# Optimization experiments

Measured on AMD Instinct MI355X. Metric: run time of the kernel, lower is better.

## Reference

```python
import jax, jax.numpy as jnp
import numpy as np


def _gcn_conv(x, W, b, src, dst, n):
    """PyG GCNConv: linear transform, then symmetric-normalized scatter-add.
    src/dst already include self-loops. deg computed over dst (col), matching PyG."""
    h = x @ W                                           # [N, C_out]
    deg = jax.ops.segment_sum(jnp.ones(dst.shape, h.dtype), dst, num_segments=n)
    dinv = jnp.where(deg > 0, deg ** -0.5, 0.0)         # deg^-1/2, inf -> 0
    norm = dinv[src] * dinv[dst]                        # [E+N]
    msg = h[src] * norm[:, None]                        # gather + scale
    return jax.ops.segment_sum(msg, dst, num_segments=n) + b


def setup_inputs() -> dict:
    key = jax.random.key(0)
    k1, k2, k3, k4 = jax.random.split(key, 4)
    N, E, F_IN, F_HID, F_OUT = 100000, 1600000, 128, 128, 128
    x = jax.random.normal(k1, (N, F_IN), dtype=jnp.float32)
    W1 = jax.random.normal(k2, (F_IN, F_HID), dtype=jnp.float32) * (1.0 / np.sqrt(F_IN))
    b1 = jnp.zeros((F_HID,), dtype=jnp.float32)
    W2 = jax.random.normal(k3, (F_HID, F_OUT), dtype=jnp.float32) * (1.0 / np.sqrt(F_HID))
    b2 = jnp.zeros((F_OUT,), dtype=jnp.float32)
    edge_index = jax.random.randint(k4, (2, E), 0, N, dtype=jnp.int64)
    return {"x": x, "W1": W1, "b1": b1, "W2": W2, "b2": b2, "edge_index": edge_index}


def reference(x, W1, b1, W2, b2, edge_index):
    n = x.shape[0]
    loops = jnp.arange(n, dtype=edge_index.dtype)       # add self-loops (PyG default)
    src = jnp.concatenate([edge_index[0], loops])
    dst = jnp.concatenate([edge_index[1], loops])
    h = jax.nn.relu(_gcn_conv(x, W1, b1, src, dst, n))
    out = jax.nn.relu(_gcn_conv(h, W2, b2, src, dst, n))
    return out
```

## Files before the change

kernel.cpp:

```cpp
#include <hip/hip_runtime.h>

#define TPB 256
#define CHA 8192

typedef _Float16 half_t;
typedef _Float16 half4 __attribute__((ext_vector_type(4)));
typedef _Float16 half8 __attribute__((ext_vector_type(8)));
typedef float f32x4 __attribute__((ext_vector_type(4)));

__global__ __launch_bounds__(512) void k_binA(unsigned* __restrict__ keys,
                                              int* __restrict__ bcursor,
                                              const int* __restrict__ ei,
                                              long long E, int NB, int CAP) {
  __shared__ int hist[512];
  __shared__ int scanv[512];
  __shared__ int base_run[512];
  __shared__ int bump[512];
  __shared__ unsigned stage[CHA];

  const int tid = threadIdx.x;
  const long long e0 = (long long)blockIdx.x * CHA;
  const int cnt_here = (int)min((long long)CHA, E - e0);

  hist[tid] = 0; bump[tid] = 0;
  __syncthreads();

  for (int i = tid; i < cnt_here; i += 512)
    atomicAdd(&hist[ei[E + e0 + i] >> 8], 1);
  __syncthreads();

  int v = hist[tid];
  scanv[tid] = v;
  __syncthreads();
  for (int ofs = 1; ofs < 512; ofs <<= 1) {
    int t = (tid >= ofs) ? scanv[tid - ofs] : 0;
    __syncthreads();
    scanv[tid] += t;
    __syncthreads();
  }
  scanv[tid] -= v;
  if (tid < NB) {
    int c = hist[tid];
    base_run[tid] = c ? atomicAdd(&bcursor[tid], c) : 0;
  }
  __syncthreads();

  for (int i = tid; i < cnt_here; i += 512) {
    int s = ei[e0 + i];
    int d = ei[E + e0 + i];
    int b = d >> 8;
    int r = atomicAdd(&bump[b], 1);
    stage[scanv[b] + r] = ((unsigned)s << 8) | (unsigned)(d & 255);
  }
  __syncthreads();

  const int wave = tid >> 6, lane = tid & 63;
  for (int b = wave; b < NB; b += 8) {
    int s0 = scanv[b], c = hist[b], rb = base_run[b];
    long long gbase = (long long)b * CAP + rb;
    int cmax = min(c, CAP - rb);
    for (int j = lane; j < cmax; j += 64) keys[gbase + j] = stage[s0 + j];
  }
}

__global__ __launch_bounds__(TPB) void k_binB(int* __restrict__ pay,
                                              int* __restrict__ cnt,
                                              int* __restrict__ off,
                                              float* __restrict__ dinv,
                                              const unsigned* __restrict__ keys,
                                              const int* __restrict__ bcursor,
                                              int N, int CAP) {
  __shared__ int lcnt[256], lofs[256], lcur[256];
  const int tid = threadIdx.x;
  const int b = blockIdx.x;
  const long long lo = (long long)b * CAP;
  const int total = min(bcursor[b], CAP);

  lcnt[tid] = 0; lcur[tid] = 0;
  __syncthreads();
  for (int i = tid; i < total; i += TPB)
    atomicAdd(&lcnt[keys[lo + i] & 255], 1);
  __syncthreads();

  int v = lcnt[tid];
  lofs[tid] = v;
  __syncthreads();
  for (int ofs = 1; ofs < 256; ofs <<= 1) {
    int t = (tid >= ofs) ? lofs[tid - ofs] : 0;
    __syncthreads();
    lofs[tid] += t;
    __syncthreads();
  }
  lofs[tid] -= v;
  __syncthreads();

  const int node = (b << 8) + tid;
  if (node < N) {
    cnt[node] = v;
    off[node] = (int)lo + lofs[tid];
    dinv[node] = rsqrtf(1.0f + (float)v);
  }

  for (int i = tid; i < total; i += TPB) {
    unsigned k = keys[lo + i];
    int l = (int)(k & 255u);
    int r = atomicAdd(&lcur[l], 1);
    pay[lo + lofs[l] + r] = (int)(k >> 8);
  }
}

__global__ __launch_bounds__(TPB) void k_prepW(half_t* __restrict__ Wf1,
                                               const float* __restrict__ W1,
                                               half_t* __restrict__ Wf2,
                                               const float* __restrict__ W2) {
  int gid = blockIdx.x * TPB + threadIdx.x;
  int f = gid & 4095;
  const float* W = (gid < 4096) ? W1 : W2;
  half_t* Wf = (gid < 4096) ? Wf1 : Wf2;
  int j0 = (f & 1) * 4;
  int lane = (f >> 1) & 63;
  int nt = (f >> 7) & 7;
  int kc = f >> 10;
  int n = nt * 16 + (lane & 15);
  int kb = kc * 32 + ((lane >> 4) << 3) + j0;
  half4 o;
  o.x = (_Float16)W[(kb + 0) * 128 + n];
  o.y = (_Float16)W[(kb + 1) * 128 + n];
  o.z = (_Float16)W[(kb + 2) * 128 + n];
  o.w = (_Float16)W[(kb + 3) * 128 + n];
  *(half4*)&Wf[f * 4] = o;
}

template <int AF16>
__global__ __launch_bounds__(TPB) void k_gemm_mfma(const void* __restrict__ Ain,
                                                   const half_t* __restrict__ Wf,
                                                   const float* __restrict__ dinv,
                                                   half_t* __restrict__ hs, int N) {
  __shared__ half_t As[128 * 128];
  __shared__ half_t Ws[16384];
  const int tid = threadIdx.x;
  const long long row0 = (long long)blockIdx.x * 128;

  {
    half8* d = (half8*)Ws;
    const half8* s = (const half8*)Wf;
#pragma unroll
    for (int i = 0; i < 8; ++i) d[i * 256 + tid] = s[i * 256 + tid];
  }
  {
#pragma unroll
    for (int i = 0; i < 8; ++i) {
      int s = i * 256 + tid;
      int lane6 = s & 63;
      int grp = s >> 6;
      int mtile = grp >> 2, kc = grp & 3;
      int m = lane6 & 15, kg = lane6 >> 4;
      long long gr = row0 + mtile * 16 + m;
      half8 hv = {};
      if (gr < (long long)N) {
        if (AF16) {
          hv = ((const half8*)Ain)[gr * 16 + kc * 4 + kg];
        } else {
          const float4* A4 = (const float4*)Ain;
          float4 v0 = A4[gr * 32 + kc * 8 + kg * 2];
          float4 v1 = A4[gr * 32 + kc * 8 + kg * 2 + 1];
          hv[0] = (_Float16)v0.x; hv[1] = (_Float16)v0.y;
          hv[2] = (_Float16)v0.z; hv[3] = (_Float16)v0.w;
          hv[4] = (_Float16)v1.x; hv[5] = (_Float16)v1.y;
          hv[6] = (_Float16)v1.z; hv[7] = (_Float16)v1.w;
        }
      }
      ((half8*)As)[s] = hv;
    }
  }
  __syncthreads();

  const int rg = tid >> 6, lane = tid & 63;
  f32x4 acc0[8], acc1[8];
#pragma unroll
  for (int nt = 0; nt < 8; ++nt) {
    f32x4 z = {0.f, 0.f, 0.f, 0.f};
    acc0[nt] = z; acc1[nt] = z;
  }
#pragma unroll
  for (int kc = 0; kc < 4; ++kc) {
    half8 a0 = ((const half8*)As)[((rg * 2 + 0) * 4 + kc) * 64 + lane];
    half8 a1 = ((const half8*)As)[((rg * 2 + 1) * 4 + kc) * 64 + lane];
#pragma unroll
    for (int nt = 0; nt < 8; ++nt) {
      half8 b = ((const half8*)Ws)[(kc * 8 + nt) * 64 + lane];
      acc0[nt] = __builtin_amdgcn_mfma_f32_16x16x32_f16(a0, b, acc0[nt], 0, 0, 0);
      acc1[nt] = __builtin_amdgcn_mfma_f32_16x16x32_f16(a1, b, acc1[nt], 0, 0, 0);
    }
  }

  const int ncol = lane & 15;
  const int mbase = (lane >> 4) << 2;
#pragma unroll
  for (int mt = 0; mt < 2; ++mt) {
#pragma unroll
    for (int r = 0; r < 4; ++r) {
      long long grow = row0 + (rg * 2 + mt) * 16 + mbase + r;
      if (grow < (long long)N) {
        float sc = dinv[grow];
        half_t* dst = &hs[grow * 128 + ncol];
#pragma unroll
        for (int nt = 0; nt < 8; ++nt)
          dst[nt * 16] =
              (_Float16)(((mt == 0) ? acc0[nt][r] : acc1[nt][r]) * sc);
      }
    }
  }
}

template <int OUTF16>
__global__ __launch_bounds__(TPB) void k_agg(void* __restrict__ outp,
                                             const half4* __restrict__ hs,
                                             const int* __restrict__ pay,
                                             const int* __restrict__ off,
                                             const int* __restrict__ cnt,
                                             const float* __restrict__ dinv,
                                             const float4* __restrict__ b, int N) {
  long long t = (long long)blockIdx.x * TPB + threadIdx.x;
  int g = (int)(t >> 5);
  if (g >= N) return;
  int c = (int)(t & 31);
  float di = dinv[g];
  float4 bv = b[c];

  half4 hv = hs[(long long)g * 32 + c];
  float4 acc;
  acc.x = (float)hv.x; acc.y = (float)hv.y;
  acc.z = (float)hv.z; acc.w = (float)hv.w;

  int p = off[g];
  const int en = p + cnt[g];

  for (; p + 8 <= en; p += 8) {
    int s[8];
#pragma unroll
    for (int u = 0; u < 8; ++u) s[u] = pay[p + u];
    half4 v[8];
#pragma unroll
    for (int u = 0; u < 8; ++u) v[u] = hs[(long long)s[u] * 32 + c];
#pragma unroll
    for (int u = 0; u < 8; ++u) {
      acc.x += (float)v[u].x; acc.y += (float)v[u].y;
      acc.z += (float)v[u].z; acc.w += (float)v[u].w;
    }
  }
  if (p + 4 <= en) {
    int s[4];
#pragma unroll
    for (int u = 0; u < 4; ++u) s[u] = pay[p + u];
    half4 v[4];
#pragma unroll
    for (int u = 0; u < 4; ++u) v[u] = hs[(long long)s[u] * 32 + c];
#pragma unroll
    for (int u = 0; u < 4; ++u) {
      acc.x += (float)v[u].x; acc.y += (float)v[u].y;
      acc.z += (float)v[u].z; acc.w += (float)v[u].w;
    }
    p += 4;
  }
  for (; p < en; ++p) {
    half4 v = hs[(long long)pay[p] * 32 + c];
    acc.x += (float)v.x; acc.y += (float)v.y;
    acc.z += (float)v.z; acc.w += (float)v.w;
  }

  float4 o;
  o.x = fmaxf(fmaf(acc.x, di, bv.x), 0.f);
  o.y = fmaxf(fmaf(acc.y, di, bv.y), 0.f);
  o.z = fmaxf(fmaf(acc.z, di, bv.z), 0.f);
  o.w = fmaxf(fmaf(acc.w, di, bv.w), 0.f);

  if (OUTF16) {
    half4 ho;
    ho.x = (_Float16)o.x; ho.y = (_Float16)o.y;
    ho.z = (_Float16)o.z; ho.w = (_Float16)o.w;
    ((half4*)outp)[(long long)g * 32 + c] = ho;
  } else {
    ((float4*)outp)[(long long)g * 32 + c] = o;
  }
}


extern "C" void kernel_launch(void* const* d_in, const int* in_sizes, int n_in,
                              void* d_out, int out_size, void* d_ws, size_t ws_size,
                              hipStream_t stream) {
  const float* x  = (const float*)d_in[0];
  const float* W1 = (const float*)d_in[1];
  const float* b1 = (const float*)d_in[2];
  const float* W2 = (const float*)d_in[3];
  const float* b2 = (const float*)d_in[4];
  const int*   ei = (const int*)d_in[5];

  const int N = in_sizes[0] / 128;
  const long long E = in_sizes[5] / 2;
  const int NB = (N + 255) >> 8;

  int CAP = (int)(((2 * (E / NB) + 255) / 256) * 256);
  if (CAP < 4096) CAP = 4096;

  char* w = (char*)d_ws;
  half_t*   hs      = (half_t*)w;          w += (size_t)N * 128 * 2;
  half_t*   a1h     = (half_t*)w;          w += (size_t)N * 128 * 2;
  int*      pay     = (int*)w;             w += (size_t)NB * CAP * 4;
  unsigned* keys    = (unsigned*)w;        w += (size_t)NB * CAP * 4;
  int*      cnt     = (int*)w;             w += (size_t)N * 4;
  int*      off     = (int*)w;             w += (size_t)N * 4;
  float*    dinv    = (float*)w;           w += (size_t)N * 4;
  half_t*   Wf1     = (half_t*)w;          w += 16384 * 2;
  half_t*   Wf2     = (half_t*)w;          w += 16384 * 2;
  int*      bcursor = (int*)w;

  float* out = (float*)d_out;

  const long long n32 = (long long)N * 32;
  const int gN32 = (int)((n32 + TPB - 1) / TPB);
  const int gGemm = (N + 127) / 128;
  const int gBinA = (int)((E + CHA - 1) / CHA);

  k_prepW<<<32, TPB, 0, stream>>>(Wf1, W1, Wf2, W2);

  hipMemsetAsync(bcursor, 0, (size_t)NB * 4, stream);
  k_binA<<<gBinA, 512, 0, stream>>>(keys, bcursor, ei, E, NB, CAP);
  k_binB<<<NB, TPB, 0, stream>>>(pay, cnt, off, dinv, keys, bcursor, N, CAP);

  k_gemm_mfma<0><<<gGemm, TPB, 0, stream>>>(x, Wf1, dinv, hs, N);
  k_agg<1><<<gN32, TPB, 0, stream>>>(a1h, (const half4*)hs, pay, off,
                                     cnt, dinv, (const float4*)b1, N);

  k_gemm_mfma<1><<<gGemm, TPB, 0, stream>>>(a1h, Wf2, dinv, hs, N);
  k_agg<0><<<gN32, TPB, 0, stream>>>(out, (const half4*)hs, pay, off,
                                     cnt, dinv, (const float4*)b2, N);
}
```

Measured before the change: 211.9 us.

## Fuse weight prep into binning, drop LDS staging, add nontemporal loads/stores

Merges the weight-conversion kernel into the edge-binning kernel as extra blocks, which removes one launch. The binning kernel no longer does the shared-memory prefix scan and staging; each edge key is written straight to its global bucket slot. Nontemporal loads and stores are added on streaming data in binB, the GEMM input read, and the aggregation kernel, so that streamed data does not evict the reused hs gather rows from cache. Writing keys directly trades coalesced writes for scattered ones, and dropping the large LDS buffer should allow more binA blocks per CU.

```diff
diff --git a/kernel.cpp b/kernel.cpp
--- a/kernel.cpp
+++ b/kernel.cpp
@@ -11,14 +11,38 @@
 __global__ __launch_bounds__(512) void k_binA(unsigned* __restrict__ keys,
                                               int* __restrict__ bcursor,
                                               const int* __restrict__ ei,
-                                              long long E, int NB, int CAP) {
+                                              long long E, int NB, int CAP,
+                                              int gBinA,
+                                              half_t* __restrict__ Wf1,
+                                              const float* __restrict__ W1,
+                                              half_t* __restrict__ Wf2,
+                                              const float* __restrict__ W2) {
+  const int tid = threadIdx.x;
+
+  if (blockIdx.x >= gBinA) {
+    int gid = (blockIdx.x - gBinA) * 512 + tid;
+    int f = gid & 4095;
+    const float* W = (gid < 4096) ? W1 : W2;
+    half_t* Wf = (gid < 4096) ? Wf1 : Wf2;
+    int j0 = (f & 1) * 4;
+    int lane = (f >> 1) & 63;
+    int nt = (f >> 7) & 7;
+    int kc = f >> 10;
+    int n = nt * 16 + (lane & 15);
+    int kb = kc * 32 + ((lane >> 4) << 3) + j0;
+    half4 o;
+    o.x = (_Float16)W[(kb + 0) * 128 + n];
+    o.y = (_Float16)W[(kb + 1) * 128 + n];
+    o.z = (_Float16)W[(kb + 2) * 128 + n];
+    o.w = (_Float16)W[(kb + 3) * 128 + n];
+    *(half4*)&Wf[f * 4] = o;
+    return;
+  }
+
   __shared__ int hist[512];
-  __shared__ int scanv[512];
   __shared__ int base_run[512];
   __shared__ int bump[512];
-  __shared__ unsigned stage[CHA];
-
-  const int tid = threadIdx.x;
+
   const long long e0 = (long long)blockIdx.x * CHA;
   const int cnt_here = (int)min((long long)CHA, E - e0);
 
@@ -29,16 +53,6 @@
     atomicAdd(&hist[ei[E + e0 + i] >> 8], 1);
   __syncthreads();
 
-  int v = hist[tid];
-  scanv[tid] = v;
-  __syncthreads();
-  for (int ofs = 1; ofs < 512; ofs <<= 1) {
-    int t = (tid >= ofs) ? scanv[tid - ofs] : 0;
-    __syncthreads();
-    scanv[tid] += t;
-    __syncthreads();
-  }
-  scanv[tid] -= v;
   if (tid < NB) {
     int c = hist[tid];
     base_run[tid] = c ? atomicAdd(&bcursor[tid], c) : 0;
@@ -49,17 +63,9 @@
     int s = ei[e0 + i];
     int d = ei[E + e0 + i];
     int b = d >> 8;
-    int r = atomicAdd(&bump[b], 1);
-    stage[scanv[b] + r] = ((unsigned)s << 8) | (unsigned)(d & 255);
-  }
-  __syncthreads();
-
-  const int wave = tid >> 6, lane = tid & 63;
-  for (int b = wave; b < NB; b += 8) {
-    int s0 = scanv[b], c = hist[b], rb = base_run[b];
-    long long gbase = (long long)b * CAP + rb;
-    int cmax = min(c, CAP - rb);
-    for (int j = lane; j < cmax; j += 64) keys[gbase + j] = stage[s0 + j];
+    int r = base_run[b] + atomicAdd(&bump[b], 1);
+    if (r < CAP)
+      keys[(long long)b * CAP + r] = ((unsigned)s << 8) | (unsigned)(d & 255);
   }
 }
 
@@ -79,7 +85,7 @@
   lcnt[tid] = 0; lcur[tid] = 0;
   __syncthreads();
   for (int i = tid; i < total; i += TPB)
-    atomicAdd(&lcnt[keys[lo + i] & 255], 1);
+    atomicAdd(&lcnt[__builtin_nontemporal_load(&keys[lo + i]) & 255], 1);
   __syncthreads();
 
   int v = lcnt[tid];
@@ -107,28 +113,6 @@
     int r = atomicAdd(&lcur[l], 1);
     pay[lo + lofs[l] + r] = (int)(k >> 8);
   }
-}
-
-__global__ __launch_bounds__(TPB) void k_prepW(half_t* __restrict__ Wf1,
-                                               const float* __restrict__ W1,
-                                               half_t* __restrict__ Wf2,
-                                               const float* __restrict__ W2) {
-  int gid = blockIdx.x * TPB + threadIdx.x;
-  int f = gid & 4095;
-  const float* W = (gid < 4096) ? W1 : W2;
-  half_t* Wf = (gid < 4096) ? Wf1 : Wf2;
-  int j0 = (f & 1) * 4;
-  int lane = (f >> 1) & 63;
-  int nt = (f >> 7) & 7;
-  int kc = f >> 10;
-  int n = nt * 16 + (lane & 15);
-  int kb = kc * 32 + ((lane >> 4) << 3) + j0;
-  half4 o;
-  o.x = (_Float16)W[(kb + 0) * 128 + n];
-  o.y = (_Float16)W[(kb + 1) * 128 + n];
-  o.z = (_Float16)W[(kb + 2) * 128 + n];
-  o.w = (_Float16)W[(kb + 3) * 128 + n];
-  *(half4*)&Wf[f * 4] = o;
 }
 
 template <int AF16>
@@ -161,13 +145,14 @@
         if (AF16) {
           hv = ((const half8*)Ain)[gr * 16 + kc * 4 + kg];
         } else {
-          const float4* A4 = (const float4*)Ain;
-          float4 v0 = A4[gr * 32 + kc * 8 + kg * 2];
-          float4 v1 = A4[gr * 32 + kc * 8 + kg * 2 + 1];
-          hv[0] = (_Float16)v0.x; hv[1] = (_Float16)v0.y;
-          hv[2] = (_Float16)v0.z; hv[3] = (_Float16)v0.w;
-          hv[4] = (_Float16)v1.x; hv[5] = (_Float16)v1.y;
-          hv[6] = (_Float16)v1.z; hv[7] = (_Float16)v1.w;
+          const f32x4* A4 = (const f32x4*)Ain;
+          f32x4 v0 = __builtin_nontemporal_load(&A4[gr * 32 + kc * 8 + kg * 2]);
+          f32x4 v1 =
+              __builtin_nontemporal_load(&A4[gr * 32 + kc * 8 + kg * 2 + 1]);
+          hv[0] = (_Float16)v0[0]; hv[1] = (_Float16)v0[1];
+          hv[2] = (_Float16)v0[2]; hv[3] = (_Float16)v0[3];
+          hv[4] = (_Float16)v1[0]; hv[5] = (_Float16)v1[1];
+          hv[6] = (_Float16)v1[2]; hv[7] = (_Float16)v1[3];
         }
       }
       ((half8*)As)[s] = hv;
@@ -220,18 +205,18 @@
                                              const int* __restrict__ off,
                                              const int* __restrict__ cnt,
                                              const float* __restrict__ dinv,
-                                             const float4* __restrict__ b, int N) {
+                                             const float* __restrict__ b, int N) {
   long long t = (long long)blockIdx.x * TPB + threadIdx.x;
   int g = (int)(t >> 5);
   if (g >= N) return;
   int c = (int)(t & 31);
   float di = dinv[g];
-  float4 bv = b[c];
+  f32x4 bv = *(const f32x4*)&b[c * 4];
 
   half4 hv = hs[(long long)g * 32 + c];
-  float4 acc;
-  acc.x = (float)hv.x; acc.y = (float)hv.y;
-  acc.z = (float)hv.z; acc.w = (float)hv.w;
+  f32x4 acc;
+  acc[0] = (float)hv.x; acc[1] = (float)hv.y;
+  acc[2] = (float)hv.z; acc[3] = (float)hv.w;
 
   int p = off[g];
   const int en = p + cnt[g];
@@ -239,49 +224,49 @@
   for (; p + 8 <= en; p += 8) {
     int s[8];
 #pragma unroll
-    for (int u = 0; u < 8; ++u) s[u] = pay[p + u];
+    for (int u = 0; u < 8; ++u) s[u] = __builtin_nontemporal_load(&pay[p + u]);
     half4 v[8];
 #pragma unroll
     for (int u = 0; u < 8; ++u) v[u] = hs[(long long)s[u] * 32 + c];
 #pragma unroll
     for (int u = 0; u < 8; ++u) {
-      acc.x += (float)v[u].x; acc.y += (float)v[u].y;
-      acc.z += (float)v[u].z; acc.w += (float)v[u].w;
+      acc[0] += (float)v[u].x; acc[1] += (float)v[u].y;
+      acc[2] += (float)v[u].z; acc[3] += (float)v[u].w;
     }
   }
   if (p + 4 <= en) {
     int s[4];
 #pragma unroll
-    for (int u = 0; u < 4; ++u) s[u] = pay[p + u];
+    for (int u = 0; u < 4; ++u) s[u] = __builtin_nontemporal_load(&pay[p + u]);
     half4 v[4];
 #pragma unroll
     for (int u = 0; u < 4; ++u) v[u] = hs[(long long)s[u] * 32 + c];
 #pragma unroll
     for (int u = 0; u < 4; ++u) {
-      acc.x += (float)v[u].x; acc.y += (float)v[u].y;
-      acc.z += (float)v[u].z; acc.w += (float)v[u].w;
+      acc[0] += (float)v[u].x; acc[1] += (float)v[u].y;
+      acc[2] += (float)v[u].z; acc[3] += (float)v[u].w;
     }
     p += 4;
   }
   for (; p < en; ++p) {
-    half4 v = hs[(long long)pay[p] * 32 + c];
-    acc.x += (float)v.x; acc.y += (float)v.y;
-    acc.z += (float)v.z; acc.w += (float)v.w;
-  }
-
-  float4 o;
-  o.x = fmaxf(fmaf(acc.x, di, bv.x), 0.f);
-  o.y = fmaxf(fmaf(acc.y, di, bv.y), 0.f);
-  o.z = fmaxf(fmaf(acc.z, di, bv.z), 0.f);
-  o.w = fmaxf(fmaf(acc.w, di, bv.w), 0.f);
+    half4 v = hs[(long long)__builtin_nontemporal_load(&pay[p]) * 32 + c];
+    acc[0] += (float)v.x; acc[1] += (float)v.y;
+    acc[2] += (float)v.z; acc[3] += (float)v.w;
+  }
+
+  f32x4 o;
+  o[0] = fmaxf(fmaf(acc[0], di, bv[0]), 0.f);
+  o[1] = fmaxf(fmaf(acc[1], di, bv[1]), 0.f);
+  o[2] = fmaxf(fmaf(acc[2], di, bv[2]), 0.f);
+  o[3] = fmaxf(fmaf(acc[3], di, bv[3]), 0.f);
 
   if (OUTF16) {
     half4 ho;
-    ho.x = (_Float16)o.x; ho.y = (_Float16)o.y;
-    ho.z = (_Float16)o.z; ho.w = (_Float16)o.w;
-    ((half4*)outp)[(long long)g * 32 + c] = ho;
+    ho.x = (_Float16)o[0]; ho.y = (_Float16)o[1];
+    ho.z = (_Float16)o[2]; ho.w = (_Float16)o[3];
+    __builtin_nontemporal_store(ho, &((half4*)outp)[(long long)g * 32 + c]);
   } else {
-    ((float4*)outp)[(long long)g * 32 + c] = o;
+    __builtin_nontemporal_store(o, &((f32x4*)outp)[(long long)g * 32 + c]);
   }
 }
 
@@ -322,17 +307,16 @@
   const int gGemm = (N + 127) / 128;
   const int gBinA = (int)((E + CHA - 1) / CHA);
 
-  k_prepW<<<32, TPB, 0, stream>>>(Wf1, W1, Wf2, W2);
-
-  hipMemsetAsync(bcursor, 0, (size_t)NB * 4, stream);
-  k_binA<<<gBinA, 512, 0, stream>>>(keys, bcursor, ei, E, NB, CAP);
+  (void)hipMemsetAsync(bcursor, 0, (size_t)NB * 4, stream);
+  k_binA<<<gBinA + 16, 512, 0, stream>>>(keys, bcursor, ei, E, NB, CAP, gBinA,
+                                         Wf1, W1, Wf2, W2);
   k_binB<<<NB, TPB, 0, stream>>>(pay, cnt, off, dinv, keys, bcursor, N, CAP);
 
   k_gemm_mfma<0><<<gGemm, TPB, 0, stream>>>(x, Wf1, dinv, hs, N);
   k_agg<1><<<gN32, TPB, 0, stream>>>(a1h, (const half4*)hs, pay, off,
-                                     cnt, dinv, (const float4*)b1, N);
+                                     cnt, dinv, b1, N);
 
   k_gemm_mfma<1><<<gGemm, TPB, 0, stream>>>(a1h, Wf2, dinv, hs, N);
   k_agg<0><<<gN32, TPB, 0, stream>>>(out, (const half4*)hs, pay, off,
-                                     cnt, dinv, (const float4*)b2, N);
-}
+                                     cnt, dinv, b2, N);
+}
```

Result: slower. 225.2 us (+6.3%).
